# Performance work log

Hardware: AMD Instinct MI355X
Metric: run time of the kernel (lower is better)

The kernel has to match this reference:

```python
import jax, jax.numpy as jnp
import numpy as np
import math

B, N, SEEDS, DIM, H = 16, 2048, 4, 512, 8
DS = DIM // H
EPS = 1e-5
LOG_2PI = math.log(2.0 * math.pi)


def setup_inputs() -> dict:
    key = jax.random.key(0)
    ks = jax.random.split(key, 12)
    s = 1.0 / math.sqrt(DIM)
    d = {}
    d["X"] = jax.random.normal(ks[0], (B, N, SEEDS, DIM), jnp.float32)
    # seed parameters (kaiming/xavier-ish init)
    d["M"] = jax.random.uniform(ks[1], (1, SEEDS, DIM), jnp.float32, -s, s) * math.sqrt(6.0)
    d["S"] = jax.random.uniform(ks[2], (1, SEEDS, DIM), jnp.float32, -s, s) * math.sqrt(6.0)
    d["p"] = jax.random.uniform(ks[3], (1, SEEDS), jnp.float32, -0.5, 0.5)
    # linear layers (PyTorch Linear: y = x @ W.T + b)
    d["Wk"] = jax.random.uniform(ks[4], (DIM, DIM), jnp.float32, -s, s)
    d["bk"] = jax.random.uniform(ks[5], (DIM,), jnp.float32, -s, s)
    d["Wv"] = jax.random.uniform(ks[6], (DIM, DIM), jnp.float32, -s, s)
    d["bv"] = jax.random.uniform(ks[7], (DIM,), jnp.float32, -s, s)
    d["Wo"] = jax.random.uniform(ks[8], (DIM, DIM), jnp.float32, -s, s)
    d["bo"] = jax.random.uniform(ks[9], (DIM,), jnp.float32, -s, s)
    # batchnorm affine params (init: weight=1, bias=0)
    d["g0"] = jnp.ones((SEEDS * DIM,), jnp.float32)
    d["b0"] = jnp.zeros((SEEDS * DIM,), jnp.float32)
    d["g1"] = jnp.ones((SEEDS * DIM,), jnp.float32)
    d["b1"] = jnp.zeros((SEEDS * DIM,), jnp.float32)
    return d


def _batchnorm(x, g, b):
    # BatchNorm1d in training mode: batch stats (biased variance), eps=1e-5
    m = x.mean(axis=0)
    v = x.var(axis=0)
    return g * (x - m) / jnp.sqrt(v + EPS) + b


def reference(X, M, S, p, Wk, bk, Wv, bv, Wo, bo, g0, b0, g1, b1):
    mu = M[0].reshape(SEEDS, H, DS)                      # [S,H,DS] per-head seeds
    sigma = jax.nn.softplus(S[0]).reshape(SEEDS, H, DS)  # [S,H,DS]
    logp = jnp.log(jax.nn.softmax(p[0], axis=-1))        # [S]

    K = (X @ Wk.T + bk).reshape(B, N, SEEDS, H, DS)
    V = (X @ Wv.T + bv).reshape(B, N, SEEDS, H, DS)

    # GMM log-likelihood scores: sum over per-head feature dim
    diff = K - mu                                        # [B,N,S,H,DS]
    ll = (-0.5 * LOG_2PI - jnp.log(sigma) - 0.5 * diff * diff / (sigma * sigma)).sum(-1)
    ll = ll + logp[:, None]                              # [B,N,S,H]

    A = jax.nn.softmax(ll / math.sqrt(DIM), axis=1)      # softmax over instances n
    O = mu + jnp.einsum('bnsh,bnshd->bshd', A, V)        # [B,S,H,DS]
    O = O.reshape(B, SEEDS, DIM)                         # head-major feature concat

    O = _batchnorm(O.reshape(B, SEEDS * DIM), g0, b0).reshape(B, SEEDS, DIM)
    O = O + jax.nn.relu(O @ Wo.T + bo)
    O = _batchnorm(O.reshape(B, SEEDS * DIM), g1, b1).reshape(B, SEEDS, DIM)
    return O
```

## Files before the change

kernel.cpp:

```cpp
#include <hip/hip_runtime.h>
#include <hip/hip_bf16.h>

typedef __attribute__((ext_vector_type(4))) float f32x4;
typedef __attribute__((ext_vector_type(8))) short bf16x8;

constexpr int NB = 16, NN = 2048, NS = 4, NDIM = 512, NH = 8, NDS = 64;
constexpr float LOG2PI = 1.8378770664093453f;
constexpr float INV_SQRT_DIM = 0.04419417382415922f;

__device__ inline short f2bf(float f) {
  __hip_bfloat16 h = __float2bfloat16(f);
  return *reinterpret_cast<short*>(&h);
}
__device__ inline float bf2f(short b) {
  union { unsigned u; float f; } v;
  v.u = ((unsigned)(unsigned short)b) << 16;
  return v.f;
}

__device__ inline void gld16(const void* g, void* l) {
  __builtin_amdgcn_global_load_lds(
      (const __attribute__((address_space(1))) void*)g,
      (__attribute__((address_space(3))) void*)l, 16, 0, 0);
}

__global__ __launch_bounds__(256) void prep_kernel(
    const float* __restrict__ Wv, float* __restrict__ WvT,
    const float* __restrict__ Wk, short* __restrict__ Wkb,
    const float* __restrict__ Mp, const float* __restrict__ Sp,
    const float* __restrict__ pp, const float* __restrict__ bkp,
    float4* __restrict__ gmm, float* __restrict__ lp2)
{
  const int blk = blockIdx.x;
  const int tid = threadIdx.x;
  if (blk < 1024) {
    const int idx = blk * 256 + tid;
    const int d = idx & 63;
    const int i = (idx >> 6) & 511;
    const int h = idx >> 15;
    WvT[idx] = Wv[(size_t)(h * 64 + d) * 512 + i];
  } else if (blk < 1152) {
    const int j = (blk - 1024) * 256 + tid;
    const float4 a = reinterpret_cast<const float4*>(Wk)[(size_t)j * 2];
    const float4 b = reinterpret_cast<const float4*>(Wk)[(size_t)j * 2 + 1];
    bf16x8 o;
    o[0] = f2bf(a.x); o[1] = f2bf(a.y); o[2] = f2bf(a.z); o[3] = f2bf(a.w);
    o[4] = f2bf(b.x); o[5] = f2bf(b.y); o[6] = f2bf(b.z); o[7] = f2bf(b.w);
    *reinterpret_cast<bf16x8*>(&Wkb[(size_t)j * 8]) = o;
  } else {
    const int idx = (blk - 1152) * 256 + tid;
    const int Jg = idx & 511;
    const float sv = Sp[idx];
    const float sig = log1pf(expf(sv));
    float4 o;
    o.x = Mp[idx];
    o.y = (-0.5f * LOG2PI - logf(sig)) * INV_SQRT_DIM;
    o.z = (0.5f / (sig * sig)) * INV_SQRT_DIM;
    o.w = bkp[Jg];
    gmm[idx] = o;
    if (idx < 4) {
      const float p0 = pp[0], p1 = pp[1], p2 = pp[2], p3 = pp[3];
      const float pmx = fmaxf(fmaxf(p0, p1), fmaxf(p2, p3));
      const float lse = pmx + logf(expf(p0 - pmx) + expf(p1 - pmx) +
                                   expf(p2 - pmx) + expf(p3 - pmx));
      lp2[idx] = (pp[idx] - lse) * INV_SQRT_DIM;
    }
  }
}

__global__ __launch_bounds__(256) void kproj1_kernel(
    const float* __restrict__ X, const short* __restrict__ Wkb,
    const float4* __restrict__ gmm, const float* __restrict__ lp2,
    float* __restrict__ ll_ws, short* __restrict__ Xb)
{
  __shared__ short As[2][128 * 64];
  __shared__ short Bs[2][128 * 64];

  const int bid0 = blockIdx.x;
  const int mt = (bid0 & 7) * 128 + (bid0 >> 3);
  const int m0 = mt * 128;
  const int c0 = 0;

  const int t = threadIdx.x;
  const int l = t & 63;
  const int w = t >> 6;
  const int wr = w >> 1, wc = w & 1;
  const int lg = l >> 4, lr = l & 15;

  f32x4 acc[4][4] = {};

  const int g8 = (l & 7) ^ (l >> 3);
  const size_t gba = (size_t)(c0 + w * 32 + (l >> 3)) * NDIM + g8 * 8;
  const int dB = (w * 32) * 64;
  auto stageB = [&](int buf, int ts) {
    const int k0 = ts << 6;
    #pragma unroll
    for (int q = 0; q < 4; ++q)
      gld16(&Wkb[gba + (size_t)(q * 8) * NDIM + k0], (char*)&Bs[buf][dB + q * 8 * 64]);
  };

  float4 rA[4][2];
  auto issueA = [&](int ts) {
    const int k0 = ts << 6;
    #pragma unroll
    for (int u = 0; u < 4; ++u) {
      const int bc = u * 256 + t;
      const int row = bc >> 3, c = bc & 7;
      const float* src = &X[(size_t)(m0 + row) * NDIM + k0 + c * 8];
      rA[u][0] = *reinterpret_cast<const float4*>(src);
      rA[u][1] = *reinterpret_cast<const float4*>(src + 4);
    }
  };
  auto cvtWriteA = [&](int buf, int ts) {
    const int k0 = ts << 6;
    #pragma unroll
    for (int u = 0; u < 4; ++u) {
      const int bc = u * 256 + t;
      const int row = bc >> 3, c = bc & 7;
      bf16x8 o;
      o[0] = f2bf(rA[u][0].x); o[1] = f2bf(rA[u][0].y);
      o[2] = f2bf(rA[u][0].z); o[3] = f2bf(rA[u][0].w);
      o[4] = f2bf(rA[u][1].x); o[5] = f2bf(rA[u][1].y);
      o[6] = f2bf(rA[u][1].z); o[7] = f2bf(rA[u][1].w);
      *reinterpret_cast<bf16x8*>(
          (char*)&As[buf][0] + row * 128 + ((c ^ (row & 7)) << 4)) = o;
      *reinterpret_cast<bf16x8*>(&Xb[(size_t)(m0 + row) * NDIM + k0 + c * 8]) = o;
    }
  };

  auto compute = [&](int buf) {
    #pragma unroll
    for (int kk = 0; kk < 64; kk += 32) {
      bf16x8 a[4], b[4];
      #pragma unroll
      for (int i = 0; i < 4; ++i) {
        const int r = wr * 64 + i * 16 + lr;
        const int byte = r * 128 + ((((kk >> 3) + lg) ^ (lr & 7)) << 4);
        a[i] = *reinterpret_cast<const bf16x8*>((const char*)&As[buf][0] + byte);
      }
      #pragma unroll
      for (int j = 0; j < 4; ++j) {
        const int r = wc * 64 + j * 16 + lr;
        const int byte = r * 128 + ((((kk >> 3) + lg) ^ (lr & 7)) << 4);
        b[j] = *reinterpret_cast<const bf16x8*>((const char*)&Bs[buf][0] + byte);
      }
      #pragma unroll
      for (int i = 0; i < 4; ++i) {
        #pragma unroll
        for (int j = 0; j < 4; ++j)
          acc[i][j] = __builtin_amdgcn_mfma_f32_16x16x32_bf16(a[i], b[j], acc[i][j], 0, 0, 0);
      }
    }
  };

  issueA(0);
  cvtWriteA(0, 0);
  stageB(0, 0);
  issueA(1);
  asm volatile("s_waitcnt vmcnt(8)" ::: "memory");
  asm volatile("s_waitcnt lgkmcnt(0)" ::: "memory");
  __builtin_amdgcn_s_barrier();
  __builtin_amdgcn_sched_barrier(0);
  for (int ts = 0; ts < 7; ++ts) {
    cvtWriteA((ts + 1) & 1, ts + 1);
    stageB((ts + 1) & 1, ts + 1);
    if (ts < 6) issueA(ts + 2);
    asm volatile("s_waitcnt lgkmcnt(0)" ::: "memory");
    __builtin_amdgcn_s_barrier();
    compute(ts & 1);
    __builtin_amdgcn_s_barrier();
  }
  asm volatile("s_waitcnt vmcnt(0)" ::: "memory");
  __builtin_amdgcn_s_barrier();
  compute(1);
  __builtin_amdgcn_sched_barrier(0);

  const float l0 = lp2[0], l1 = lp2[1], l2 = lp2[2], l3 = lp2[3];
  const float lpv[4] = {l0, l1, l2, l3};

  float part[4][4];
  #pragma unroll
  for (int i = 0; i < 4; ++i)
    #pragma unroll
    for (int e = 0; e < 4; ++e) part[i][e] = 0.f;

  #pragma unroll
  for (int j = 0; j < 4; ++j) {
    const int Jg = c0 + wc * 64 + j * 16 + lr;
    #pragma unroll
    for (int e = 0; e < 4; ++e) {
      const float4 gw = gmm[e * NDIM + Jg];
      #pragma unroll
      for (int i = 0; i < 4; ++i) {
        const float kv = acc[i][j][e] + gw.w;
        const float d = kv - gw.x;
        part[i][e] += gw.y - d * d * gw.z;
      }
    }
  }
  #pragma unroll
  for (int off = 1; off < 16; off <<= 1) {
    #pragma unroll
    for (int i = 0; i < 4; ++i)
      #pragma unroll
      for (int e = 0; e < 4; ++e)
        part[i][e] += __shfl_xor(part[i][e], off, 64);
  }
  if (lr == 0) {
    const int h = wc;
    #pragma unroll
    for (int i = 0; i < 4; ++i) {
      #pragma unroll
      for (int e = 0; e < 4; ++e) {
        const int R = m0 + wr * 64 + i * 16 + 4 * lg + e;
        const int bn = R >> 2;
        const int bb = bn >> 11;
        const int nn = bn & (NN - 1);
        ll_ws[((size_t)((bb * NS + e) * NH + h)) * NN + nn] = part[i][e] + lpv[e];
      }
    }
  }
}

__global__ __launch_bounds__(256) void kproj2_kernel(
    const short* __restrict__ Xb, const short* __restrict__ Wkb,
    const float4* __restrict__ gmm, const float* __restrict__ lp2,
    float* __restrict__ ll_ws)
{
  __shared__ short As[2][128 * 64];
  __shared__ short Bs[2][128 * 64];

  const int bid0 = blockIdx.x;
  const int xcd = bid0 & 7;
  const int q = bid0 >> 3;
  const int mt = xcd * 128 + q / 3;
  const int ct = 1 + q % 3;
  const int m0 = mt * 128;
  const int c0 = ct * 128;

  const int t = threadIdx.x;
  const int l = t & 63;
  const int w = t >> 6;
  const int wr = w >> 1, wc = w & 1;
  const int lg = l >> 4, lr = l & 15;

  f32x4 acc[4][4] = {};

  const int g8 = (l & 7) ^ (l >> 3);
  const size_t gxa = (size_t)(m0 + w * 32 + (l >> 3)) * NDIM + g8 * 8;
  const size_t gba = (size_t)(c0 + w * 32 + (l >> 3)) * NDIM + g8 * 8;
  const int dA = (w * 32) * 64;

  auto stage = [&](int buf, int ts) {
    const int k0 = ts << 6;
    #pragma unroll
    for (int qq = 0; qq < 4; ++qq) {
      const size_t so = (size_t)(qq * 8) * NDIM + k0;
      const int dd = dA + (qq * 8) * 64;
      gld16(&Xb[gxa + so],  (char*)&As[buf][dd]);
      gld16(&Wkb[gba + so], (char*)&Bs[buf][dd]);
    }
  };

  auto compute = [&](int buf) {
    #pragma unroll
    for (int kk = 0; kk < 64; kk += 32) {
      bf16x8 a[4], b[4];
      #pragma unroll
      for (int i = 0; i < 4; ++i) {
        const int r = wr * 64 + i * 16 + lr;
        const int byte = r * 128 + ((((kk >> 3) + lg) ^ (lr & 7)) << 4);
        a[i] = *reinterpret_cast<const bf16x8*>((const char*)&As[buf][0] + byte);
      }
      #pragma unroll
      for (int j = 0; j < 4; ++j) {
        const int r = wc * 64 + j * 16 + lr;
        const int byte = r * 128 + ((((kk >> 3) + lg) ^ (lr & 7)) << 4);
        b[j] = *reinterpret_cast<const bf16x8*>((const char*)&Bs[buf][0] + byte);
      }
      #pragma unroll
      for (int i = 0; i < 4; ++i) {
        #pragma unroll
        for (int j = 0; j < 4; ++j)
          acc[i][j] = __builtin_amdgcn_mfma_f32_16x16x32_bf16(a[i], b[j], acc[i][j], 0, 0, 0);
      }
    }
  };

  stage(0, 0);
  __builtin_amdgcn_sched_barrier(0);
  for (int ts = 0; ts < 7; ++ts) {
    stage((ts + 1) & 1, ts + 1);
    asm volatile("s_waitcnt vmcnt(8)" ::: "memory");
    __builtin_amdgcn_s_barrier();
    compute(ts & 1);
    __builtin_amdgcn_s_barrier();
  }
  asm volatile("s_waitcnt vmcnt(0)" ::: "memory");
  __builtin_amdgcn_s_barrier();
  compute(1);
  __builtin_amdgcn_sched_barrier(0);

  const float l0 = lp2[0], l1 = lp2[1], l2 = lp2[2], l3 = lp2[3];
  const float lpv[4] = {l0, l1, l2, l3};

  float part[4][4];
  #pragma unroll
  for (int i = 0; i < 4; ++i)
    #pragma unroll
    for (int e = 0; e < 4; ++e) part[i][e] = 0.f;

  #pragma unroll
  for (int j = 0; j < 4; ++j) {
    const int Jg = c0 + wc * 64 + j * 16 + lr;
    #pragma unroll
    for (int e = 0; e < 4; ++e) {
      const float4 gw = gmm[e * NDIM + Jg];
      #pragma unroll
      for (int i = 0; i < 4; ++i) {
        const float kv = acc[i][j][e] + gw.w;
        const float d = kv - gw.x;
        part[i][e] += gw.y - d * d * gw.z;
      }
    }
  }
  #pragma unroll
  for (int off = 1; off < 16; off <<= 1) {
    #pragma unroll
    for (int i = 0; i < 4; ++i)
      #pragma unroll
      for (int e = 0; e < 4; ++e)
        part[i][e] += __shfl_xor(part[i][e], off, 64);
  }
  if (lr == 0) {
    const int h = ct * 2 + wc;
    #pragma unroll
    for (int i = 0; i < 4; ++i) {
      #pragma unroll
      for (int e = 0; e < 4; ++e) {
        const int R = m0 + wr * 64 + i * 16 + 4 * lg + e;
        const int bn = R >> 2;
        const int bb = bn >> 11;
        const int nn = bn & (NN - 1);
        ll_ws[((size_t)((bb * NS + e) * NH + h)) * NN + nn] = part[i][e] + lpv[e];
      }
    }
  }
}

__global__ __launch_bounds__(256) void y_kernel(
    const float* __restrict__ ll_ws, const short* __restrict__ Xb,
    float* __restrict__ Yp, float2* __restrict__ msws)
{
  __shared__ float wT[256][8];
  __shared__ float redm[8][4];
  __shared__ float reds[8][4];
  const int blk = blockIdx.x;
  const int bs = blk & 63;
  const int nq = blk >> 6;
  const int b = bs >> 2, s = bs & 3;
  const int g0 = bs * 8;
  const int t = threadIdx.x;
  const int w = t >> 6, l = t & 63;

  float lv[8];
  #pragma unroll
  for (int h = 0; h < 8; ++h) {
    lv[h] = ll_ws[(size_t)(g0 + h) * NN + nq * 256 + t];
    float mm = lv[h];
    #pragma unroll
    for (int off = 1; off < 64; off <<= 1) mm = fmaxf(mm, __shfl_xor(mm, off, 64));
    if (l == 0) redm[h][w] = mm;
  }
  __syncthreads();
  float mx[8];
  #pragma unroll
  for (int h = 0; h < 8; ++h) {
    mx[h] = fmaxf(fmaxf(redm[h][0], redm[h][1]), fmaxf(redm[h][2], redm[h][3]));
    const float e = expf(lv[h] - mx[h]);
    wT[t][h] = e;
    float ss = e;
    #pragma unroll
    for (int off = 1; off < 64; off <<= 1) ss += __shfl_xor(ss, off, 64);
    if (l == 0) reds[h][w] = ss;
  }
  __syncthreads();
  if (t < 8) {
    const float sum = reds[t][0] + reds[t][1] + reds[t][2] + reds[t][3];
    msws[(size_t)(g0 + t) * 8 + nq] = make_float2(mx[t], sum);
  }

  const ushort2* X2 = reinterpret_cast<const ushort2*>(Xb);
  const size_t xbase = ((size_t)(b * 2048 + nq * 256) * 4 + s) * 256 + t;
  float acc[8][2] = {};
  #pragma unroll 4
  for (int n = 0; n < 256; ++n) {
    const ushort2 xv = X2[xbase + (size_t)n * 1024];
    const float x0 = bf2f((short)xv.x), x1 = bf2f((short)xv.y);
    const float4 w0 = *reinterpret_cast<const float4*>(&wT[n][0]);
    const float4 w1 = *reinterpret_cast<const float4*>(&wT[n][4]);
    acc[0][0] += w0.x * x0; acc[0][1] += w0.x * x1;
    acc[1][0] += w0.y * x0; acc[1][1] += w0.y * x1;
    acc[2][0] += w0.z * x0; acc[2][1] += w0.z * x1;
    acc[3][0] += w0.w * x0; acc[3][1] += w0.w * x1;
    acc[4][0] += w1.x * x0; acc[4][1] += w1.x * x1;
    acc[5][0] += w1.y * x0; acc[5][1] += w1.y * x1;
    acc[6][0] += w1.z * x0; acc[6][1] += w1.z * x1;
    acc[7][0] += w1.w * x0; acc[7][1] += w1.w * x1;
  }
  #pragma unroll
  for (int h = 0; h < 8; ++h) {
    float* yp = Yp + ((size_t)((nq * 64 + bs) * 8 + h)) * 512 + 2 * t;
    yp[0] = acc[h][0]; yp[1] = acc[h][1];
  }
}

__global__ __launch_bounds__(256) void poolproj_kernel(
    const float* __restrict__ Yp, const float2* __restrict__ msws,
    const float* __restrict__ WvT, const float* __restrict__ bvp,
    const float* __restrict__ Mp, float* __restrict__ O0)
{
  __shared__ float ys[512];
  __shared__ float pr[4][64];
  const int g = blockIdx.x;
  const int bs = g >> 3, h = g & 7;
  const int s = bs & 3;
  const int t = threadIdx.x;

  const float2* msp = msws + (size_t)g * 8;
  float M = -1e30f;
  #pragma unroll
  for (int q = 0; q < 8; ++q) M = fmaxf(M, msp[q].x);
  float cq[8];
  float S = 0.f;
  #pragma unroll
  for (int q = 0; q < 8; ++q) {
    cq[q] = expf(msp[q].x - M);
    S += msp[q].y * cq[q];
  }
  const float rS = 1.f / S;

  float a0 = 0.f, a1 = 0.f;
  #pragma unroll
  for (int q = 0; q < 8; ++q) {
    const float* yp = Yp + ((size_t)((q * 64 + bs) * 8 + h)) * 512;
    const float c = cq[q] * rS;
    a0 += yp[t] * c;
    a1 += yp[t + 256] * c;
  }
  ys[t] = a0; ys[t + 256] = a1;
  __syncthreads();

  const int d = t & 63, p = t >> 6;
  const float* wt = WvT + ((size_t)h * 512 + p * 128) * 64 + d;
  const float* yy = ys + p * 128;
  float acc = 0.f;
  #pragma unroll 4
  for (int i = 0; i < 128; ++i) acc += yy[i] * wt[(size_t)i * 64];
  pr[p][d] = acc;
  __syncthreads();
  if (t < 64) {
    const float tot = pr[0][t] + pr[1][t] + pr[2][t] + pr[3][t];
    O0[(size_t)g * 64 + t] = Mp[s * NDIM + h * NDS + t] + bvp[h * 64 + t] + tot;
  }
}

__global__ __launch_bounds__(256) void bnmlp_kernel(
    const float* __restrict__ O0, const float* __restrict__ gg,
    const float* __restrict__ bb, const float* __restrict__ Wo,
    const float* __restrict__ bo, float* __restrict__ Zo)
{
  __shared__ float ys[512];
  const int blk = blockIdx.x;
  const int t = threadIdx.x;
  const int r = blk >> 1;
  const int b = r >> 2, s = r & 3;

  #pragma unroll
  for (int u = 0; u < 2; ++u) {
    const int i = u * 256 + t;
    const int f = s * 512 + i;
    float x[NB];
    float m = 0.f;
    #pragma unroll
    for (int bq = 0; bq < NB; ++bq) { x[bq] = O0[bq * 2048 + f]; m += x[bq]; }
    m *= (1.f / NB);
    float v = 0.f;
    #pragma unroll
    for (int bq = 0; bq < NB; ++bq) { const float d = x[bq] - m; v += d * d; }
    v *= (1.f / NB);
    const float inv = rsqrtf(v + 1e-5f) * gg[f];
    ys[i] = (x[b] - m) * inv + bb[f];
  }
  __syncthreads();

  const int j = ((blk & 1) << 8) + t;
  const float4* yv = reinterpret_cast<const float4*>(ys);
  const float4* wrow = reinterpret_cast<const float4*>(Wo + (size_t)j * NDIM);
  float acc = 0.f;
  #pragma unroll 4
  for (int i = 0; i < 128; ++i) {
    const float4 a = yv[i], w = wrow[i];
    acc += a.x * w.x + a.y * w.y + a.z * w.z + a.w * w.w;
  }
  Zo[(size_t)r * 512 + j] = ys[j] + fmaxf(acc + bo[j], 0.f);
}

__global__ __launch_bounds__(256) void bn_kernel(
    const float* __restrict__ Xin, const float* __restrict__ gg,
    const float* __restrict__ bb, float* __restrict__ Yo)
{
  const int f = blockIdx.x * 256 + threadIdx.x;
  float x[NB];
  float m = 0.f;
  #pragma unroll
  for (int b = 0; b < NB; ++b) { x[b] = Xin[b * (NS * NDIM) + f]; m += x[b]; }
  m *= (1.f / NB);
  float v = 0.f;
  #pragma unroll
  for (int b = 0; b < NB; ++b) { const float d = x[b] - m; v += d * d; }
  v *= (1.f / NB);
  const float inv = rsqrtf(v + 1e-5f) * gg[f];
  const float bf = bb[f];
  #pragma unroll
  for (int b = 0; b < NB; ++b) Yo[b * (NS * NDIM) + f] = (x[b] - m) * inv + bf;
}

extern "C" void kernel_launch(void* const* d_in, const int* in_sizes, int n_in,
                              void* d_out, int out_size, void* d_ws, size_t ws_size,
                              hipStream_t stream) {
  (void)in_sizes; (void)n_in; (void)out_size; (void)ws_size;
  const float* X  = (const float*)d_in[0];
  const float* M  = (const float*)d_in[1];
  const float* S  = (const float*)d_in[2];
  const float* p  = (const float*)d_in[3];
  const float* Wk = (const float*)d_in[4];
  const float* bk = (const float*)d_in[5];
  const float* Wv = (const float*)d_in[6];
  const float* bv = (const float*)d_in[7];
  const float* Wo = (const float*)d_in[8];
  const float* bo = (const float*)d_in[9];
  const float* g0 = (const float*)d_in[10];
  const float* b0 = (const float*)d_in[11];
  const float* g1 = (const float*)d_in[12];
  const float* b1 = (const float*)d_in[13];

  char* ws = (char*)d_ws;
  short* Xb    = (short*)ws;
  float* ll_ws = (float*)(ws + (size_t)134217728);
  float* Yp    = (float*)(ws + (size_t)138416128);
  float* O0    = (float*)(ws + (size_t)146804736);
  float* Z     = (float*)(ws + (size_t)147066880);
  short* Wkb   = (short*)(ws + (size_t)147197952);
  float* WvT   = (float*)(ws + (size_t)147722240);
  float4* gmm  = (float4*)(ws + (size_t)148770816);
  float* lp2   = (float*)(ws + (size_t)148803584);
  float2* msws = (float2*)(ws + (size_t)148803712);

  prep_kernel<<<1160, 256, 0, stream>>>(Wv, WvT, Wk, Wkb, M, S, p, bk, gmm, lp2);
  kproj1_kernel<<<1024, 256, 0, stream>>>(X, Wkb, gmm, lp2, ll_ws, Xb);
  kproj2_kernel<<<3072, 256, 0, stream>>>(Xb, Wkb, gmm, lp2, ll_ws);
  y_kernel<<<512, 256, 0, stream>>>(ll_ws, Xb, Yp, msws);
  poolproj_kernel<<<512, 256, 0, stream>>>(Yp, msws, WvT, bv, M, O0);
  bnmlp_kernel<<<128, 256, 0, stream>>>(O0, g0, b0, Wo, bo, Z);
  bn_kernel<<<8, 256, 0, stream>>>(Z, g1, b1, (float*)d_out);
}
```

Before: 236.3 us.

## Split y_kernel instance loop across waves with 16-byte loads and LDS reduction

The weighted pooling loop in y_kernel now gives each wave a quarter of the 256 instances, with each lane loading 8 contiguous bf16 features (16 bytes) instead of 2. Partial sums are then reduced across the four waves through shared memory, one head at a time. The goal is wider, better-coalesced global loads and more independent memory requests in flight. The cost is 64 accumulators per thread, which raises register pressure, plus extra LDS traffic and 16 barriers for the reduction.

```diff
diff --git a/kernel.cpp b/kernel.cpp
--- a/kernel.cpp
+++ b/kernel.cpp
@@ -355,6 +355,7 @@
   __shared__ float wT[256][8];
   __shared__ float redm[8][4];
   __shared__ float reds[8][4];
+  __shared__ float red[4][8][64];
   const int blk = blockIdx.x;
   const int bs = blk & 63;
   const int nq = blk >> 6;
@@ -390,28 +391,39 @@
     msws[(size_t)(g0 + t) * 8 + nq] = make_float2(mx[t], sum);
   }
 
-  const ushort2* X2 = reinterpret_cast<const ushort2*>(Xb);
-  const size_t xbase = ((size_t)(b * 2048 + nq * 256) * 4 + s) * 256 + t;
-  float acc[8][2] = {};
-  #pragma unroll 4
-  for (int n = 0; n < 256; ++n) {
-    const ushort2 xv = X2[xbase + (size_t)n * 1024];
-    const float x0 = bf2f((short)xv.x), x1 = bf2f((short)xv.y);
-    const float4 w0 = *reinterpret_cast<const float4*>(&wT[n][0]);
-    const float4 w1 = *reinterpret_cast<const float4*>(&wT[n][4]);
-    acc[0][0] += w0.x * x0; acc[0][1] += w0.x * x1;
-    acc[1][0] += w0.y * x0; acc[1][1] += w0.y * x1;
-    acc[2][0] += w0.z * x0; acc[2][1] += w0.z * x1;
-    acc[3][0] += w0.w * x0; acc[3][1] += w0.w * x1;
-    acc[4][0] += w1.x * x0; acc[4][1] += w1.x * x1;
-    acc[5][0] += w1.y * x0; acc[5][1] += w1.y * x1;
-    acc[6][0] += w1.z * x0; acc[6][1] += w1.z * x1;
-    acc[7][0] += w1.w * x0; acc[7][1] += w1.w * x1;
-  }
-  #pragma unroll
+  float acc[8][8] = {};
+  const size_t rowbase =
+      ((size_t)(b * 2048 + nq * 256) * 4 + s) * 512 + (size_t)l * 8;
+  #pragma unroll 2
+  for (int i = 0; i < 64; ++i) {
+    const int nl = w * 64 + i;
+    const bf16x8 xv = *reinterpret_cast<const bf16x8*>(
+        &Xb[rowbase + (size_t)nl * 2048]);
+    float x[8];
+    #pragma unroll
+    for (int j = 0; j < 8; ++j) x[j] = bf2f(xv[j]);
+    const float4 w0 = *reinterpret_cast<const float4*>(&wT[nl][0]);
+    const float4 w1 = *reinterpret_cast<const float4*>(&wT[nl][4]);
+    const float wh[8] = {w0.x, w0.y, w0.z, w0.w, w1.x, w1.y, w1.z, w1.w};
+    #pragma unroll
+    for (int h = 0; h < 8; ++h)
+      #pragma unroll
+      for (int j = 0; j < 8; ++j) acc[h][j] += wh[h] * x[j];
+  }
+
+  #pragma unroll 1
   for (int h = 0; h < 8; ++h) {
-    float* yp = Yp + ((size_t)((nq * 64 + bs) * 8 + h)) * 512 + 2 * t;
-    yp[0] = acc[h][0]; yp[1] = acc[h][1];
+    __syncthreads();
+    #pragma unroll
+    for (int j = 0; j < 8; ++j) red[w][j][l] = acc[h][j];
+    __syncthreads();
+    float* yp = Yp + ((size_t)((nq * 64 + bs) * 8 + h)) * 512;
+    #pragma unroll
+    for (int u = 0; u < 2; ++u) {
+      const int d = u * 256 + t;
+      const int jj = d & 7, ll2 = d >> 3;
+      yp[d] = red[0][jj][ll2] + red[1][jj][ll2] + red[2][jj][ll2] + red[3][jj][ll2];
+    }
   }
 }
 
```

After: 243.6 us. 1.03x slower.
